# Optimization experiments

Hardware: AMD Instinct MI355X
Metric: run time of the kernel (lower is better)

Reference implementation:

```python
import jax, jax.numpy as jnp
import numpy as np

B, S, H, I, E, TOP_K = 2, 2048, 1024, 2048, 8, 2


def setup_inputs() -> dict:
    key = jax.random.key(0)
    k1, k2, k3, k4, k5 = jax.random.split(key, 5)
    scale_h = 1.0 / np.sqrt(H)
    scale_i = 1.0 / np.sqrt(I)
    return {
        "hidden_states": jax.random.normal(k1, (B, S, H), dtype=jnp.float32),
        "router_w": jax.random.normal(k2, (H, E), dtype=jnp.float32) * scale_h,
        "gate_w": jax.random.normal(k3, (E, H, I), dtype=jnp.float32) * scale_h,
        "up_w": jax.random.normal(k4, (E, H, I), dtype=jnp.float32) * scale_h,
        "out_w": jax.random.normal(k5, (E, I, H), dtype=jnp.float32) * scale_i,
    }


def reference(hidden_states, router_w, gate_w, up_w, out_w):
    b, s, h = hidden_states.shape
    x = hidden_states.reshape(-1, h)  # [T, H], T = B*S

    # Router: logits -> softmax -> top-k -> renormalize -> dense routing matrix
    router_logits = x @ router_w  # [T, E]
    router_probs = jax.nn.softmax(router_logits, axis=-1)
    top_p, top_i = jax.lax.top_k(router_probs, TOP_K)  # [T, K]
    top_p = top_p / jnp.sum(top_p, axis=-1, keepdims=True)
    one_hot = jax.nn.one_hot(top_i, E, dtype=top_p.dtype)  # [T, K, E]
    routing_full = jnp.sum(one_hot * top_p[..., None], axis=1)  # [T, E]
    routing_full = routing_full.T  # [E, T]

    # Dense all-expert FFN (SwiGLU), as in the original batched einsum form
    gate = jnp.einsum("th,ehm->etm", x, gate_w)  # [E, T, I]
    gate = jax.nn.silu(gate)
    intermediate = jnp.einsum("th,ehm->etm", x, up_w)  # [E, T, I]
    hidden = intermediate * gate
    expert_out = jnp.einsum("eti,eih->eth", hidden, out_w)  # [E, T, H]

    # Weighted combine over experts
    out = jnp.sum(expert_out * routing_full[:, :, None], axis=0)  # [T, H]
    out = out.reshape(b, s, h)
    return out, router_logits
```

## Files before the change

### kernel.cpp

```cpp
#include <hip/hip_runtime.h>
#include <hip/hip_bf16.h>
#include <stdint.h>

#define TT 4096
#define HH 1024
#define II 2048
#define EE 8
#define RB 16

typedef short bf16x8 __attribute__((ext_vector_type(8)));
typedef float f32x4 __attribute__((ext_vector_type(4)));

__device__ __forceinline__ unsigned short f2bf(float f) {
  unsigned u = __float_as_uint(f);
  u += 0x7FFF + ((u >> 16) & 1);
  return (unsigned short)(u >> 16);
}

__device__ __forceinline__ void gl_lds16(const void* g, void* l) {
  auto gp = reinterpret_cast<const __attribute__((address_space(1))) unsigned int*>(
      reinterpret_cast<uintptr_t>(g));
  auto lp = reinterpret_cast<__attribute__((address_space(3))) unsigned int*>(
      reinterpret_cast<uintptr_t>(l));
  __builtin_amdgcn_global_load_lds(gp, lp, 16, 0, 0);
}

__global__ void prep_kernel(const float* __restrict__ gw, const float* __restrict__ uw,
                            const float* __restrict__ ow,
                            unsigned short* __restrict__ gwt, unsigned short* __restrict__ uwt,
                            unsigned short* __restrict__ owt) {
  __shared__ unsigned int tl[64 * 32];
  int z = blockIdx.z;
  int which = z >> 3, e = z & 7;
  const float* in; unsigned short* out; int M, N;
  if (which == 0)      { in = gw; out = gwt; M = HH; N = II; }
  else if (which == 1) { in = uw; out = uwt; M = HH; N = II; }
  else                 { in = ow; out = owt; M = II; N = HH; }
  int nb = N / 64;
  int bx = blockIdx.x % nb, by = blockIdx.x / nb;
  size_t base = (size_t)e * M * N;
  int mB = by * 64, nB = bx * 64;
  int tid = threadIdx.x;

  union F4 { float4 v; float f[4]; };
  int c4 = (tid & 15) * 4;
  int mp = tid >> 4;
#pragma unroll
  for (int it = 0; it < 2; ++it) {
    int m = (mp + it * 16) * 2;
    const float* p0 = in + base + (size_t)(mB + m) * N + nB + c4;
    F4 a, b;
    a.v = *(const float4*)p0;
    b.v = *(const float4*)(p0 + N);
    int mdw = m >> 1;
#pragma unroll
    for (int i = 0; i < 4; ++i) {
      int n = c4 + i;
      unsigned v = (unsigned)f2bf(a.f[i]) | ((unsigned)f2bf(b.f[i]) << 16);
      tl[n * 32 + ((mdw + n) & 31)] = v;
    }
  }
  __syncthreads();
  int n2 = tid >> 3;
  int md8 = (tid & 7) * 4;
#pragma unroll
  for (int it = 0; it < 2; ++it) {
    int n = n2 + it * 32;
    unsigned vv[4];
#pragma unroll
    for (int i = 0; i < 4; ++i)
      vv[i] = tl[n * 32 + ((md8 + i + n) & 31)];
    uint4 o4 = make_uint4(vv[0], vv[1], vv[2], vv[3]);
    *(uint4*)(out + base + (size_t)(nB + n) * M + mB + md8 * 2) = o4;
  }
}

__global__ void router_kernel(const float* __restrict__ x, const float* __restrict__ rw,
                              float* __restrict__ logits_out, int* __restrict__ cnt,
                              int* __restrict__ list, int* __restrict__ tslot,
                              float2* __restrict__ tw, unsigned short* __restrict__ xb) {
  __shared__ int bcnt[EE];
  __shared__ int bbase[EE];
  __shared__ int te[RB][2];
  int tid = threadIdx.x, wave = tid >> 6, lane = tid & 63;
  if (tid < EE) bcnt[tid] = 0;
  __syncthreads();
  int t0 = blockIdx.x * RB;

  for (int sub = 0; sub < RB / 4; ++sub) {
    int li = sub * 4 + wave;
    int t = t0 + li;
    float acc[EE];
#pragma unroll
    for (int e = 0; e < EE; ++e) acc[e] = 0.f;
#pragma unroll
    for (int j = 0; j < 4; ++j) {
      int h = j * 256 + lane * 4;
      union F4 { float4 v; float f[4]; } xv;
      xv.v = *(const float4*)(x + (size_t)t * HH + h);
      union { unsigned short s[4]; uint2 v; } pk;
#pragma unroll
      for (int i = 0; i < 4; ++i) pk.s[i] = f2bf(xv.f[i]);
      *(uint2*)(xb + (size_t)t * HH + h) = pk.v;
#pragma unroll
      for (int i = 0; i < 4; ++i) {
        const float4* r4 = (const float4*)(rw + (h + i) * EE);
        float4 r0 = r4[0], r1 = r4[1];
        float xs = xv.f[i];
        acc[0] += xs * r0.x; acc[1] += xs * r0.y; acc[2] += xs * r0.z; acc[3] += xs * r0.w;
        acc[4] += xs * r1.x; acc[5] += xs * r1.y; acc[6] += xs * r1.z; acc[7] += xs * r1.w;
      }
    }
#pragma unroll
    for (int e = 0; e < EE; ++e)
#pragma unroll
      for (int off = 32; off; off >>= 1) acc[e] += __shfl_down(acc[e], off);
    if (lane == 0) {
      float4* lo = (float4*)(logits_out + (size_t)t * EE);
      lo[0] = make_float4(acc[0], acc[1], acc[2], acc[3]);
      lo[1] = make_float4(acc[4], acc[5], acc[6], acc[7]);
      int e0 = 0; float b0 = acc[0];
#pragma unroll
      for (int e = 1; e < EE; ++e) if (acc[e] > b0) { b0 = acc[e]; e0 = e; }
      int e1 = -1; float b1 = -3.4e38f;
#pragma unroll
      for (int e = 0; e < EE; ++e) if (e != e0 && acc[e] > b1) { b1 = acc[e]; e1 = e; }
      float w0 = 1.f / (1.f + __expf(b1 - b0));
      tw[t] = make_float2(w0, 1.f - w0);
      int lp0 = atomicAdd(&bcnt[e0], 1);
      int lp1 = atomicAdd(&bcnt[e1], 1);
      te[li][0] = e0 | (lp0 << 8);
      te[li][1] = e1 | (lp1 << 8);
    }
  }
  __syncthreads();
  if (tid < EE) bbase[tid] = atomicAdd(&cnt[tid], bcnt[tid]);
  __syncthreads();
  if (tid < RB * 2) {
    int li = tid >> 1, s = tid & 1;
    int v = te[li][s];
    int e = v & 255, lp = v >> 8;
    int p = bbase[e] + lp;
    int t = t0 + li;
    list[e * TT + p] = t;
    tslot[t * 2 + s] = (e << 16) | p;
  }
}

__launch_bounds__(256, 3)
__global__ void gemm1_kernel(const unsigned short* __restrict__ xb,
                             const unsigned short* __restrict__ gwt,
                             const unsigned short* __restrict__ uwt,
                             unsigned short* __restrict__ hidden,
                             const int* __restrict__ cnt, const int* __restrict__ list) {
  int e = blockIdx.z;
  int cn = cnt[e];
  int hb0 = 0;
  for (int i = 0; i < EE; ++i) hb0 += (i < e) ? cnt[i] : 0;
  int mBase = blockIdx.y * 128;
  if (mBase >= cn) return;
  int nBase = blockIdx.x * 64;

  __shared__ __align__(16) unsigned short smem[16384];
  __shared__ int stok[128];

  int tid = threadIdx.x, wave = tid >> 6, lane = tid & 63;
  if (tid < 128) {
    int g = mBase + tid;
    stok[tid] = list[e * TT + (g < cn ? g : cn - 1)];
  }
  __syncthreads();

  const char* gaddr[8];
#pragma unroll
  for (int j = 0; j < 8; ++j) {
    int c = wave * 512 + j * 64 + lane;
    const char* g;
    if (c < 1024) {
      int r = c >> 3, sl = (c & 7) ^ (r & 7);
      g = (const char*)xb + (size_t)stok[r] * (HH * 2) + sl * 16;
    } else if (c < 1536) {
      int cc = c - 1024, r = cc >> 3, sl = (cc & 7) ^ (r & 7);
      g = (const char*)gwt + ((size_t)e * II + nBase + r) * (HH * 2) + sl * 16;
    } else {
      int cc = c - 1536, r = cc >> 3, sl = (cc & 7) ^ (r & 7);
      g = (const char*)uwt + ((size_t)e * II + nBase + r) * (HH * 2) + sl * 16;
    }
    gaddr[j] = g;
  }

  int q = lane >> 4, m16 = lane & 15;
  int wr = wave & 1, wc = wave >> 1;
  int faddrA[4][2], faddrBg[2][2], faddrBu[2][2];
#pragma unroll
  for (int mi = 0; mi < 4; ++mi) {
    int R = wr * 64 + mi * 16 + m16;
#pragma unroll
    for (int h = 0; h < 2; ++h)
      faddrA[mi][h] = (R * 8 + ((h * 4 + q) ^ (R & 7))) * 16;
  }
#pragma unroll
  for (int ni = 0; ni < 2; ++ni) {
    int n = wc * 32 + ni * 16 + m16;
#pragma unroll
    for (int h = 0; h < 2; ++h) {
      faddrBg[ni][h] = (1024 + n * 8 + ((h * 4 + q) ^ (n & 7))) * 16;
      faddrBu[ni][h] = (1536 + n * 8 + ((h * 4 + q) ^ (n & 7))) * 16;
    }
  }

  f32x4 zero4 = {0.f, 0.f, 0.f, 0.f};
  f32x4 accG[4][2], accU[4][2];
#pragma unroll
  for (int mi = 0; mi < 4; ++mi)
#pragma unroll
    for (int ni = 0; ni < 2; ++ni) { accG[mi][ni] = zero4; accU[mi][ni] = zero4; }

  const char* smemc = (const char*)smem;
  for (int kt = 0; kt < HH / 64; ++kt) {
    __syncthreads();
#pragma unroll
    for (int j = 0; j < 8; ++j) {
      gl_lds16(gaddr[j], (char*)smem + (size_t)(wave * 512 + j * 64) * 16);
      gaddr[j] += 128;
    }
    __syncthreads();
#pragma unroll
    for (int h = 0; h < 2; ++h) {
      bf16x8 aF[4], bG[2], bU[2];
#pragma unroll
      for (int mi = 0; mi < 4; ++mi) aF[mi] = *(const bf16x8*)(smemc + faddrA[mi][h]);
#pragma unroll
      for (int ni = 0; ni < 2; ++ni) {
        bG[ni] = *(const bf16x8*)(smemc + faddrBg[ni][h]);
        bU[ni] = *(const bf16x8*)(smemc + faddrBu[ni][h]);
      }
#pragma unroll
      for (int mi = 0; mi < 4; ++mi)
#pragma unroll
        for (int ni = 0; ni < 2; ++ni) {
          accG[mi][ni] = __builtin_amdgcn_mfma_f32_16x16x32_bf16(aF[mi], bG[ni], accG[mi][ni], 0, 0, 0);
          accU[mi][ni] = __builtin_amdgcn_mfma_f32_16x16x32_bf16(aF[mi], bU[ni], accU[mi][ni], 0, 0, 0);
        }
    }
  }

  int hb = hb0 + mBase;
  int rowsValid = cn - mBase; if (rowsValid > 128) rowsValid = 128;
#pragma unroll
  for (int mi = 0; mi < 4; ++mi)
#pragma unroll
    for (int ni = 0; ni < 2; ++ni)
#pragma unroll
      for (int r = 0; r < 4; ++r) {
        int row = wr * 64 + mi * 16 + q * 4 + r;
        if (row < rowsValid) {
          float g = accG[mi][ni][r], u = accU[mi][ni][r];
          float h = g / (1.f + __expf(-g)) * u;
          hidden[(size_t)(hb + row) * II + nBase + wc * 32 + ni * 16 + m16] = f2bf(h);
        }
      }
}

__launch_bounds__(256, 3)
__global__ void gemm2_kernel(const unsigned short* __restrict__ hidden,
                             const unsigned short* __restrict__ owt,
                             float* __restrict__ expert_out,
                             const int* __restrict__ cnt) {
  int e = blockIdx.z;
  int cn = cnt[e];
  int hb0 = 0;
  for (int i = 0; i < EE; ++i) hb0 += (i < e) ? cnt[i] : 0;
  int mBase = blockIdx.y * 128;
  if (mBase >= cn) return;
  int nBase = blockIdx.x * 128;

  __shared__ __align__(16) unsigned short smem[16384];

  int tid = threadIdx.x, wave = tid >> 6, lane = tid & 63;
  int hb = hb0 + mBase;
  const char* gaddr[8];
#pragma unroll
  for (int j = 0; j < 8; ++j) {
    int c = wave * 512 + j * 64 + lane;
    const char* g;
    if (c < 1024) {
      int r = c >> 3, sl = (c & 7) ^ (r & 7);
      g = (const char*)hidden + (size_t)(hb + r) * (II * 2) + sl * 16;
    } else {
      int cc = c - 1024, r = cc >> 3, sl = (cc & 7) ^ (r & 7);
      g = (const char*)owt + ((size_t)e * HH + nBase + r) * (II * 2) + sl * 16;
    }
    gaddr[j] = g;
  }

  int q = lane >> 4, m16 = lane & 15;
  int wr = wave & 1, wc = wave >> 1;
  int faddrA[4][2], faddrB[4][2];
#pragma unroll
  for (int mi = 0; mi < 4; ++mi) {
    int R = wr * 64 + mi * 16 + m16;
#pragma unroll
    for (int h = 0; h < 2; ++h)
      faddrA[mi][h] = (R * 8 + ((h * 4 + q) ^ (R & 7))) * 16;
  }
#pragma unroll
  for (int ni = 0; ni < 4; ++ni) {
    int n = wc * 64 + ni * 16 + m16;
#pragma unroll
    for (int h = 0; h < 2; ++h)
      faddrB[ni][h] = (1024 + n * 8 + ((h * 4 + q) ^ (n & 7))) * 16;
  }

  f32x4 zero4 = {0.f, 0.f, 0.f, 0.f};
  f32x4 acc[4][4];
#pragma unroll
  for (int mi = 0; mi < 4; ++mi)
#pragma unroll
    for (int ni = 0; ni < 4; ++ni) acc[mi][ni] = zero4;

  const char* smemc = (const char*)smem;
  for (int kt = 0; kt < II / 64; ++kt) {
    __syncthreads();
#pragma unroll
    for (int j = 0; j < 8; ++j) {
      gl_lds16(gaddr[j], (char*)smem + (size_t)(wave * 512 + j * 64) * 16);
      gaddr[j] += 128;
    }
    __syncthreads();
#pragma unroll
    for (int h = 0; h < 2; ++h) {
      bf16x8 aF[4], bF[4];
#pragma unroll
      for (int mi = 0; mi < 4; ++mi) aF[mi] = *(const bf16x8*)(smemc + faddrA[mi][h]);
#pragma unroll
      for (int ni = 0; ni < 4; ++ni) bF[ni] = *(const bf16x8*)(smemc + faddrB[ni][h]);
#pragma unroll
      for (int mi = 0; mi < 4; ++mi)
#pragma unroll
        for (int ni = 0; ni < 4; ++ni)
          acc[mi][ni] = __builtin_amdgcn_mfma_f32_16x16x32_bf16(aF[mi], bF[ni], acc[mi][ni], 0, 0, 0);
    }
  }

  int rowsValid = cn - mBase; if (rowsValid > 128) rowsValid = 128;
#pragma unroll
  for (int mi = 0; mi < 4; ++mi)
#pragma unroll
    for (int ni = 0; ni < 4; ++ni)
#pragma unroll
      for (int r = 0; r < 4; ++r) {
        int row = wr * 64 + mi * 16 + q * 4 + r;
        if (row < rowsValid)
          expert_out[(size_t)(hb + row) * HH + nBase + wc * 64 + ni * 16 + m16] = acc[mi][ni][r];
      }
}

__global__ void combine_kernel(const float* __restrict__ expert_out,
                               const int* __restrict__ cnt, const int* __restrict__ tslot,
                               const float2* __restrict__ tw, float* __restrict__ out) {
  int pre[EE];
  int s = 0;
#pragma unroll
  for (int e = 0; e < EE; ++e) { pre[e] = s; s += cnt[e]; }
  int t = blockIdx.x;
  int s0 = tslot[t * 2], s1 = tslot[t * 2 + 1];
  float2 w = tw[t];
  int r0 = pre[s0 >> 16] + (s0 & 0xFFFF);
  int r1 = pre[s1 >> 16] + (s1 & 0xFFFF);
  const float4* a = (const float4*)(expert_out + (size_t)r0 * HH);
  const float4* b = (const float4*)(expert_out + (size_t)r1 * HH);
  float4* o = (float4*)(out + (size_t)t * HH);
  int c = threadIdx.x;
  float4 av = a[c], bv = b[c];
  o[c] = make_float4(w.x * av.x + w.y * bv.x, w.x * av.y + w.y * bv.y,
                     w.x * av.z + w.y * bv.z, w.x * av.w + w.y * bv.w);
}

extern "C" void kernel_launch(void* const* d_in, const int* in_sizes, int n_in,
                              void* d_out, int out_size, void* d_ws, size_t ws_size,
                              hipStream_t stream) {
  (void)in_sizes; (void)n_in; (void)out_size; (void)ws_size;
  const float* x  = (const float*)d_in[0];
  const float* rw = (const float*)d_in[1];
  const float* gw = (const float*)d_in[2];
  const float* uw = (const float*)d_in[3];
  const float* ow = (const float*)d_in[4];
  float* out = (float*)d_out;
  float* logits = out + (size_t)TT * HH;

  char* ws = (char*)d_ws;
  size_t o = 0;
  auto alloc = [&](size_t bytes) {
    char* p = ws + o;
    o += (bytes + 255) & ~(size_t)255;
    return p;
  };
  unsigned short* xb  = (unsigned short*)alloc((size_t)TT * HH * 2);
  unsigned short* gwt = (unsigned short*)alloc((size_t)EE * II * HH * 2);
  unsigned short* uwt = (unsigned short*)alloc((size_t)EE * II * HH * 2);
  unsigned short* owt = (unsigned short*)alloc((size_t)EE * HH * II * 2);
  unsigned short* hidden = (unsigned short*)alloc((size_t)(2 * TT + 128) * II * 2);
  int*   cnt   = (int*)alloc(EE * 4);
  int*   list  = (int*)alloc((size_t)EE * TT * 4);
  int*   tslot = (int*)alloc((size_t)TT * 2 * 4);
  float2* tw   = (float2*)alloc((size_t)TT * 8);
  float* expert_out = (float*)gwt;

  hipMemsetAsync(cnt, 0, EE * 4, stream);

  prep_kernel<<<dim3(512, 1, 3 * EE), 256, 0, stream>>>(gw, uw, ow, gwt, uwt, owt);
  router_kernel<<<TT / RB, 256, 0, stream>>>(x, rw, logits, cnt, list, tslot, tw, xb);
  gemm1_kernel<<<dim3(II / 64, TT / 128, EE), 256, 0, stream>>>(xb, gwt, uwt, hidden, cnt, list);
  gemm2_kernel<<<dim3(HH / 128, TT / 128, EE), 256, 0, stream>>>(hidden, owt, expert_out, cnt);
  combine_kernel<<<TT, 256, 0, stream>>>(expert_out, cnt, tslot, tw, out);
}
```

Measured before the change: 409.2 us.

## Move x bf16 cast to prep kernel, pad counters, narrow gemm2 tiles

Moves the fp32-to-bf16 conversion of x out of the router into extra prep_kernel blocks (z=24..31, 8192 elements per block) and raises the router's tokens per block from 16 to 64. Pads the per-expert counters to separate cache lines to reduce atomic contention. Halves the gemm2 N tile from 128 to 64, which doubles the grid and shrinks LDS and accumulators to raise occupancy and wave count. The trade-off is less B-tile reuse per block and more redundant A loads in gemm2.

```diff
diff --git a/kernel.cpp b/kernel.cpp
--- a/kernel.cpp
+++ b/kernel.cpp
@@ -6,7 +6,8 @@
 #define HH 1024
 #define II 2048
 #define EE 8
-#define RB 16
+#define RB 64
+#define CSTRIDE 32
 
 typedef short bf16x8 __attribute__((ext_vector_type(8)));
 typedef float f32x4 __attribute__((ext_vector_type(4)));
@@ -26,12 +27,29 @@
 }
 
 __global__ void prep_kernel(const float* __restrict__ gw, const float* __restrict__ uw,
-                            const float* __restrict__ ow,
+                            const float* __restrict__ ow, const float* __restrict__ x,
                             unsigned short* __restrict__ gwt, unsigned short* __restrict__ uwt,
-                            unsigned short* __restrict__ owt) {
+                            unsigned short* __restrict__ owt, unsigned short* __restrict__ xb) {
   __shared__ unsigned int tl[64 * 32];
   int z = blockIdx.z;
   int which = z >> 3, e = z & 7;
+  int tid = threadIdx.x;
+
+  if (which == 3) {
+    size_t b0 = (size_t)blockIdx.x * 8192;
+#pragma unroll
+    for (int it = 0; it < 4; ++it) {
+      size_t i = b0 + it * 2048 + tid * 8;
+      float4 a = *(const float4*)(x + i);
+      float4 b = *(const float4*)(x + i + 4);
+      union { unsigned short s[8]; uint4 v; } o;
+      o.s[0] = f2bf(a.x); o.s[1] = f2bf(a.y); o.s[2] = f2bf(a.z); o.s[3] = f2bf(a.w);
+      o.s[4] = f2bf(b.x); o.s[5] = f2bf(b.y); o.s[6] = f2bf(b.z); o.s[7] = f2bf(b.w);
+      *(uint4*)(xb + i) = o.v;
+    }
+    return;
+  }
+
   const float* in; unsigned short* out; int M, N;
   if (which == 0)      { in = gw; out = gwt; M = HH; N = II; }
   else if (which == 1) { in = uw; out = uwt; M = HH; N = II; }
@@ -40,7 +58,6 @@
   int bx = blockIdx.x % nb, by = blockIdx.x / nb;
   size_t base = (size_t)e * M * N;
   int mB = by * 64, nB = bx * 64;
-  int tid = threadIdx.x;
 
   union F4 { float4 v; float f[4]; };
   int c4 = (tid & 15) * 4;
@@ -78,7 +95,7 @@
 __global__ void router_kernel(const float* __restrict__ x, const float* __restrict__ rw,
                               float* __restrict__ logits_out, int* __restrict__ cnt,
                               int* __restrict__ list, int* __restrict__ tslot,
-                              float2* __restrict__ tw, unsigned short* __restrict__ xb) {
+                              float2* __restrict__ tw) {
   __shared__ int bcnt[EE];
   __shared__ int bbase[EE];
   __shared__ int te[RB][2];
@@ -98,10 +115,6 @@
       int h = j * 256 + lane * 4;
       union F4 { float4 v; float f[4]; } xv;
       xv.v = *(const float4*)(x + (size_t)t * HH + h);
-      union { unsigned short s[4]; uint2 v; } pk;
-#pragma unroll
-      for (int i = 0; i < 4; ++i) pk.s[i] = f2bf(xv.f[i]);
-      *(uint2*)(xb + (size_t)t * HH + h) = pk.v;
 #pragma unroll
       for (int i = 0; i < 4; ++i) {
         const float4* r4 = (const float4*)(rw + (h + i) * EE);
@@ -134,7 +147,7 @@
     }
   }
   __syncthreads();
-  if (tid < EE) bbase[tid] = atomicAdd(&cnt[tid], bcnt[tid]);
+  if (tid < EE) bbase[tid] = atomicAdd(&cnt[tid * CSTRIDE], bcnt[tid]);
   __syncthreads();
   if (tid < RB * 2) {
     int li = tid >> 1, s = tid & 1;
@@ -154,9 +167,9 @@
                              unsigned short* __restrict__ hidden,
                              const int* __restrict__ cnt, const int* __restrict__ list) {
   int e = blockIdx.z;
-  int cn = cnt[e];
+  int cn = cnt[e * CSTRIDE];
   int hb0 = 0;
-  for (int i = 0; i < EE; ++i) hb0 += (i < e) ? cnt[i] : 0;
+  for (int i = 0; i < EE; ++i) hb0 += (i < e) ? cnt[i * CSTRIDE] : 0;
   int mBase = blockIdx.y * 128;
   if (mBase >= cn) return;
   int nBase = blockIdx.x * 64;
@@ -268,21 +281,21 @@
                              float* __restrict__ expert_out,
                              const int* __restrict__ cnt) {
   int e = blockIdx.z;
-  int cn = cnt[e];
+  int cn = cnt[e * CSTRIDE];
   int hb0 = 0;
-  for (int i = 0; i < EE; ++i) hb0 += (i < e) ? cnt[i] : 0;
+  for (int i = 0; i < EE; ++i) hb0 += (i < e) ? cnt[i * CSTRIDE] : 0;
   int mBase = blockIdx.y * 128;
   if (mBase >= cn) return;
-  int nBase = blockIdx.x * 128;
-
-  __shared__ __align__(16) unsigned short smem[16384];
+  int nBase = blockIdx.x * 64;
+
+  __shared__ __align__(16) unsigned short smem[12288];
 
   int tid = threadIdx.x, wave = tid >> 6, lane = tid & 63;
   int hb = hb0 + mBase;
-  const char* gaddr[8];
-#pragma unroll
-  for (int j = 0; j < 8; ++j) {
-    int c = wave * 512 + j * 64 + lane;
+  const char* gaddr[6];
+#pragma unroll
+  for (int j = 0; j < 6; ++j) {
+    int c = wave * 384 + j * 64 + lane;
     const char* g;
     if (c < 1024) {
       int r = c >> 3, sl = (c & 7) ^ (r & 7);
@@ -296,7 +309,7 @@
 
   int q = lane >> 4, m16 = lane & 15;
   int wr = wave & 1, wc = wave >> 1;
-  int faddrA[4][2], faddrB[4][2];
+  int faddrA[4][2], faddrB[2][2];
 #pragma unroll
   for (int mi = 0; mi < 4; ++mi) {
     int R = wr * 64 + mi * 16 + m16;
@@ -305,40 +318,40 @@
       faddrA[mi][h] = (R * 8 + ((h * 4 + q) ^ (R & 7))) * 16;
   }
 #pragma unroll
-  for (int ni = 0; ni < 4; ++ni) {
-    int n = wc * 64 + ni * 16 + m16;
+  for (int ni = 0; ni < 2; ++ni) {
+    int n = wc * 32 + ni * 16 + m16;
 #pragma unroll
     for (int h = 0; h < 2; ++h)
       faddrB[ni][h] = (1024 + n * 8 + ((h * 4 + q) ^ (n & 7))) * 16;
   }
 
   f32x4 zero4 = {0.f, 0.f, 0.f, 0.f};
-  f32x4 acc[4][4];
+  f32x4 acc[4][2];
 #pragma unroll
   for (int mi = 0; mi < 4; ++mi)
 #pragma unroll
-    for (int ni = 0; ni < 4; ++ni) acc[mi][ni] = zero4;
+    for (int ni = 0; ni < 2; ++ni) acc[mi][ni] = zero4;
 
   const char* smemc = (const char*)smem;
   for (int kt = 0; kt < II / 64; ++kt) {
     __syncthreads();
 #pragma unroll
-    for (int j = 0; j < 8; ++j) {
-      gl_lds16(gaddr[j], (char*)smem + (size_t)(wave * 512 + j * 64) * 16);
+    for (int j = 0; j < 6; ++j) {
+      gl_lds16(gaddr[j], (char*)smem + (size_t)(wave * 384 + j * 64) * 16);
       gaddr[j] += 128;
     }
     __syncthreads();
 #pragma unroll
     for (int h = 0; h < 2; ++h) {
-      bf16x8 aF[4], bF[4];
+      bf16x8 aF[4], bF[2];
 #pragma unroll
       for (int mi = 0; mi < 4; ++mi) aF[mi] = *(const bf16x8*)(smemc + faddrA[mi][h]);
 #pragma unroll
-      for (int ni = 0; ni < 4; ++ni) bF[ni] = *(const bf16x8*)(smemc + faddrB[ni][h]);
+      for (int ni = 0; ni < 2; ++ni) bF[ni] = *(const bf16x8*)(smemc + faddrB[ni][h]);
 #pragma unroll
       for (int mi = 0; mi < 4; ++mi)
 #pragma unroll
-        for (int ni = 0; ni < 4; ++ni)
+        for (int ni = 0; ni < 2; ++ni)
           acc[mi][ni] = __builtin_amdgcn_mfma_f32_16x16x32_bf16(aF[mi], bF[ni], acc[mi][ni], 0, 0, 0);
     }
   }
@@ -347,12 +360,12 @@
 #pragma unroll
   for (int mi = 0; mi < 4; ++mi)
 #pragma unroll
-    for (int ni = 0; ni < 4; ++ni)
+    for (int ni = 0; ni < 2; ++ni)
 #pragma unroll
       for (int r = 0; r < 4; ++r) {
         int row = wr * 64 + mi * 16 + q * 4 + r;
         if (row < rowsValid)
-          expert_out[(size_t)(hb + row) * HH + nBase + wc * 64 + ni * 16 + m16] = acc[mi][ni][r];
+          expert_out[(size_t)(hb + row) * HH + nBase + wc * 32 + ni * 16 + m16] = acc[mi][ni][r];
       }
 }
 
@@ -362,7 +375,7 @@
   int pre[EE];
   int s = 0;
 #pragma unroll
-  for (int e = 0; e < EE; ++e) { pre[e] = s; s += cnt[e]; }
+  for (int e = 0; e < EE; ++e) { pre[e] = s; s += cnt[e * CSTRIDE]; }
   int t = blockIdx.x;
   int s0 = tslot[t * 2], s1 = tslot[t * 2 + 1];
   float2 w = tw[t];
@@ -401,17 +414,17 @@
   unsigned short* uwt = (unsigned short*)alloc((size_t)EE * II * HH * 2);
   unsigned short* owt = (unsigned short*)alloc((size_t)EE * HH * II * 2);
   unsigned short* hidden = (unsigned short*)alloc((size_t)(2 * TT + 128) * II * 2);
-  int*   cnt   = (int*)alloc(EE * 4);
+  int*   cnt   = (int*)alloc(EE * CSTRIDE * 4);
   int*   list  = (int*)alloc((size_t)EE * TT * 4);
   int*   tslot = (int*)alloc((size_t)TT * 2 * 4);
   float2* tw   = (float2*)alloc((size_t)TT * 8);
   float* expert_out = (float*)gwt;
 
-  hipMemsetAsync(cnt, 0, EE * 4, stream);
-
-  prep_kernel<<<dim3(512, 1, 3 * EE), 256, 0, stream>>>(gw, uw, ow, gwt, uwt, owt);
-  router_kernel<<<TT / RB, 256, 0, stream>>>(x, rw, logits, cnt, list, tslot, tw, xb);
+  hipMemsetAsync(cnt, 0, EE * CSTRIDE * 4, stream);
+
+  prep_kernel<<<dim3(512, 1, 4 * EE), 256, 0, stream>>>(gw, uw, ow, x, gwt, uwt, owt, xb);
+  router_kernel<<<TT / RB, 256, 0, stream>>>(x, rw, logits, cnt, list, tslot, tw);
   gemm1_kernel<<<dim3(II / 64, TT / 128, EE), 256, 0, stream>>>(xb, gwt, uwt, hidden, cnt, list);
-  gemm2_kernel<<<dim3(HH / 128, TT / 128, EE), 256, 0, stream>>>(hidden, owt, expert_out, cnt);
+  gemm2_kernel<<<dim3(HH / 64, TT / 128, EE), 256, 0, stream>>>(hidden, owt, expert_out, cnt);
   combine_kernel<<<TT, 256, 0, stream>>>(expert_out, cnt, tslot, tw, out);
 }
```

New measurement: 462.3 us. 13.0% more time.
